# Performance work log

Measured on AMD Instinct MI355X. Metric: run time of the kernel, lower is better.

## Reference

```python
import jax, jax.numpy as jnp
import numpy as np

D_MODEL = 1024
N_HEADS = 16
D_H = D_MODEL // N_HEADS
MAX_LEN = 2048
BATCH = 2
SEQ = 2048
EPS = 1e-8
W_SCALE = 0.02


def _rms_norm(x, w):
    # RMSNorm: x * rsqrt(mean(x^2) + eps) * w
    ms = jnp.mean(jnp.square(x), axis=-1, keepdims=True)
    return w * (x * jax.lax.rsqrt(ms + EPS))


def setup_inputs() -> dict:
    key = jax.random.key(0)
    ks = jax.random.split(key, 12)
    d = D_MODEL
    inp = {
        "x": jax.random.normal(ks[0], (BATCH, SEQ, d), dtype=jnp.float32),
        "t_bias": jnp.zeros((1,), dtype=jnp.float32),  # unused by the module
        "p_bias": jax.random.normal(ks[1], (MAX_LEN, N_HEADS), dtype=jnp.float32),
        # AMS layer params (Linear stored as [in, out])
        "wq": jax.random.normal(ks[2], (d, d), dtype=jnp.float32) * W_SCALE,
        "bq": jnp.zeros((d,), dtype=jnp.float32),
        "wk": jax.random.normal(ks[3], (d, d), dtype=jnp.float32) * W_SCALE,
        "bk": jnp.zeros((d,), dtype=jnp.float32),
        "wv": jax.random.normal(ks[4], (d, d), dtype=jnp.float32) * W_SCALE,
        "bv": jnp.zeros((d,), dtype=jnp.float32),
        "wu": jax.random.normal(ks[5], (d, d), dtype=jnp.float32) * W_SCALE,
        "bu": jnp.zeros((d,), dtype=jnp.float32),
        "g_ams": jnp.ones((d,), dtype=jnp.float32),   # shared RMSNorm weight in AMSLayer
        # MFFN layer params
        "w0": jax.random.normal(ks[6], (d, d), dtype=jnp.float32) * W_SCALE,
        "b0": jnp.zeros((d,), dtype=jnp.float32),
        "w1": jax.random.normal(ks[7], (d, 2 * d), dtype=jnp.float32) * W_SCALE,
        "b1": jnp.zeros((2 * d,), dtype=jnp.float32),
        "w2": jax.random.normal(ks[8], (d, d), dtype=jnp.float32) * W_SCALE,
        "b2": jnp.zeros((d,), dtype=jnp.float32),
        "g_mffn": jnp.ones((d,), dtype=jnp.float32),
    }
    return inp


def reference(x, t_bias, p_bias, wq, bq, wk, bk, wv, bv, wu, bu, g_ams,
              w0, b0, w1, b1, w2, b2, g_mffn):
    B, S, d = x.shape
    H, dh = N_HEADS, D_H

    # ---- AMS layer ----
    x_norm = _rms_norm(x, g_ams)

    def proj(w, b):
        # [B,S,d] -> [B,H,S,dh]
        return (x_norm @ w + b).reshape(B, S, H, dh).transpose(0, 2, 1, 3)

    q = proj(wq, bq)
    k = proj(wk, bk)
    v = proj(wv, bv)

    scale = 1.0 / np.sqrt(dh).astype(np.float32)
    score = jnp.einsum('bhsd,bhtd->bhst', q, k) * scale
    # additive positional bias: p_bias[:S].T -> [H,S], broadcast over query dim
    score = score + p_bias[:S, :].T[None, :, None, :]

    attn = jax.nn.silu(score)                        # SiLU instead of softmax
    out = jnp.einsum('bhst,bhtd->bhsd', attn, v)
    out = out.transpose(0, 2, 1, 3).reshape(B, S, d)

    u = jax.nn.silu(x_norm @ wu + bu)
    ams_out = _rms_norm(out, g_ams) * u

    # ---- MFFN layer ----
    o = (ams_out @ w0 + b0) + x
    o_norm = _rms_norm(o, g_mffn)
    x12 = o_norm @ w1 + b1
    x1, x2 = jnp.split(x12, 2, axis=-1)
    swiglu = jax.nn.silu(x1) * x2
    return (swiglu @ w2 + b2) + o
```

## Files before the change

kernel.cpp:

```cpp
#include <hip/hip_runtime.h>
#include <stdint.h>
#include <math.h>


#define D    1024
#define NH   16
#define DH   64
#define B_   2
#define S_   2048
#define ROWS 4096
#define LQ   4096
#define EPSR 1e-8f

typedef unsigned short u16;
typedef __attribute__((ext_vector_type(8))) short short8;
typedef __attribute__((ext_vector_type(4))) float f32x4;
typedef __attribute__((ext_vector_type(16))) float f32x16;
typedef __attribute__((ext_vector_type(4))) int int4v;

__device__ __forceinline__ float bf2f(u16 u) {
    union { uint32_t i; float f; } c; c.i = ((uint32_t)u) << 16; return c.f;
}
__device__ __forceinline__ u16 f2bf(float f) {
    union { float f; uint32_t i; } c; c.f = f;
    uint32_t x = c.i;
    x += 0x7fffu + ((x >> 16) & 1u);
    return (u16)(x >> 16);
}
#define LOG2E 1.44269504f
__device__ __forceinline__ float silu_fast(float v) {
    return v * __builtin_amdgcn_rcpf(1.0f + __builtin_amdgcn_exp2f(v * -LOG2E));
}

__global__ __launch_bounds__(256) void transpose_all_kernel(
    const float* __restrict__ wq, const float* __restrict__ wk,
    const float* __restrict__ wv, const float* __restrict__ wu,
    const float* __restrict__ w0, const float* __restrict__ w2,
    const float* __restrict__ w1,
    u16* __restrict__ wT4, u16* __restrict__ w0T,
    u16* __restrict__ w2T, u16* __restrict__ w1T)
{
    const unsigned MI = 1u << 20;
    const int z = blockIdx.z;
    const float* W; u16* WT; int N; int noff = 0;
    switch (z) {
        case 0: W = wq; WT = wT4;          N = 1024; break;
        case 1: W = wk; WT = wT4 + 1 * MI; N = 1024; break;
        case 2: W = wv; WT = wT4 + 2 * MI; N = 1024; break;
        case 3: W = wu; WT = wT4 + 3 * MI; N = 1024; break;
        case 4: W = w0; WT = w0T;          N = 1024; break;
        case 5: W = w2; WT = w2T;          N = 1024; break;
        case 6: W = w1; WT = w1T;          N = 2048; noff = 0;    break;
        default:W = w1; WT = w1T;          N = 2048; noff = 1024; break;
    }
    __shared__ float T[64][65];
    const int tid = threadIdx.x;
    const int n0 = (blockIdx.x << 6) + noff;
    const int k0 = blockIdx.y << 6;
    const int rr = tid >> 4;
    const int cc = (tid & 15) << 2;
#pragma unroll
    for (int l = 0; l < 4; ++l) {
        const int r = rr + (l << 4);
        float4 v = *(const float4*)&W[(size_t)(k0 + r) * N + n0 + cc];
        T[cc + 0][r] = v.x; T[cc + 1][r] = v.y;
        T[cc + 2][r] = v.z; T[cc + 3][r] = v.w;
    }
    __syncthreads();
    const int n  = tid >> 2;
    const int ks = (tid & 3) << 4;
#pragma unroll
    for (int m = 0; m < 4; ++m) {
        const int k = ks + (m << 2);
        float4 v = *(const float4*)&T[n][k];
        ushort4 o;
        o.x = f2bf(v.x); o.y = f2bf(v.y); o.z = f2bf(v.z); o.w = f2bf(v.w);
        *(ushort4*)&WT[(size_t)(n0 + n) * 1024 + k0 + k] = o;
    }
}

__global__ __launch_bounds__(256) void pbt_kernel(
    const float* __restrict__ pb, float* __restrict__ pbT)
{
    const int tid = threadIdx.x;
    const int r = (blockIdx.x << 7) + (tid >> 1);
    const int c0 = (tid & 1) << 3;
    float4 v0 = *(const float4*)&pb[(size_t)r * NH + c0];
    float4 v1 = *(const float4*)&pb[(size_t)r * NH + c0 + 4];
    pbT[(size_t)(c0 + 0) * S_ + r] = v0.x;
    pbT[(size_t)(c0 + 1) * S_ + r] = v0.y;
    pbT[(size_t)(c0 + 2) * S_ + r] = v0.z;
    pbT[(size_t)(c0 + 3) * S_ + r] = v0.w;
    pbT[(size_t)(c0 + 4) * S_ + r] = v1.x;
    pbT[(size_t)(c0 + 5) * S_ + r] = v1.y;
    pbT[(size_t)(c0 + 6) * S_ + r] = v1.z;
    pbT[(size_t)(c0 + 7) * S_ + r] = v1.w;
}

__global__ __launch_bounds__(256) void rmsnorm_kernel(
    const float* __restrict__ inf, const u16* __restrict__ inb, int ldi,
    const float* __restrict__ g,
    const u16* __restrict__ mul, int ldm,
    u16* __restrict__ out, int ldo)
{
    const int row = blockIdx.x;
    const int tid = threadIdx.x;
    const int c = tid << 2;
    float x0, x1, x2, x3;
    if (inb) {
        ushort4 xi = *(const ushort4*)&inb[(size_t)row * ldi + c];
        x0 = bf2f(xi.x); x1 = bf2f(xi.y); x2 = bf2f(xi.z); x3 = bf2f(xi.w);
    } else {
        float4 xi = *(const float4*)&inf[(size_t)row * ldi + c];
        x0 = xi.x; x1 = xi.y; x2 = xi.z; x3 = xi.w;
    }
    float ss = x0*x0 + x1*x1 + x2*x2 + x3*x3;
#pragma unroll
    for (int off = 32; off > 0; off >>= 1) ss += __shfl_down(ss, off, 64);
    __shared__ float red[4];
    if ((tid & 63) == 0) red[tid >> 6] = ss;
    __syncthreads();
    float r = rsqrtf((red[0] + red[1] + red[2] + red[3]) * (1.0f / D) + EPSR);
    float4 gv = *(const float4*)&g[c];
    float v0 = x0 * r * gv.x, v1 = x1 * r * gv.y, v2 = x2 * r * gv.z, v3 = x3 * r * gv.w;
    if (mul) {
        ushort4 mi = *(const ushort4*)&mul[(size_t)row * ldm + c];
        v0 *= bf2f(mi.x); v1 *= bf2f(mi.y); v2 *= bf2f(mi.z); v3 *= bf2f(mi.w);
    }
    ushort4 o;
    o.x = f2bf(v0); o.y = f2bf(v1); o.z = f2bf(v2); o.w = f2bf(v3);
    *(ushort4*)&out[(size_t)row * ldo + c] = o;
}

__global__ __launch_bounds__(256) void gemm128(
    const u16* __restrict__ A, const u16* __restrict__ WT,
    const float* __restrict__ bs0, const float* __restrict__ bs1,
    const float* __restrict__ bs2, const float* __restrict__ bs3,
    u16* __restrict__ outb, int ldo, int actmask,
    u16* __restrict__ VT, int vtsel)
{
    __shared__ u16 As[128 * 32];
    __shared__ u16 Bs[128 * 32];
    const int tid  = threadIdx.x;
    const int wave = tid >> 6;
    const int lane = tid & 63;
    const int lm   = lane & 15;
    const int quad = lane >> 4;
    const int row0 = blockIdx.y << 7;
    const int col0 = blockIdx.x << 7;
    const int wr = (wave >> 1) << 6;
    const int wc = (wave & 1) << 6;

    const int srow = wave * 32 + (lane >> 2);
    const int skp  = (lane & 3) << 3;
    const u16* Ag = A  + (size_t)(row0 + srow) * 1024 + skp;
    const u16* Bg = WT + (size_t)(col0 + srow) * 1024 + skp;
    u16* Asd0 = &As[(wave * 32) * 32];
    u16* Asd1 = &As[(wave * 32 + 16) * 32];
    u16* Bsd0 = &Bs[(wave * 32) * 32];
    u16* Bsd1 = &Bs[(wave * 32 + 16) * 32];

    f32x4 acc[4][4] = {};

    for (int k0 = 0; k0 < 1024; k0 += 32) {
        __syncthreads();
        __builtin_amdgcn_global_load_lds(
            (const __attribute__((address_space(1))) void*)(Ag + k0),
            (__attribute__((address_space(3))) void*)Asd0, 16, 0, 0);
        __builtin_amdgcn_global_load_lds(
            (const __attribute__((address_space(1))) void*)(Ag + 16 * 1024 + k0),
            (__attribute__((address_space(3))) void*)Asd1, 16, 0, 0);
        __builtin_amdgcn_global_load_lds(
            (const __attribute__((address_space(1))) void*)(Bg + k0),
            (__attribute__((address_space(3))) void*)Bsd0, 16, 0, 0);
        __builtin_amdgcn_global_load_lds(
            (const __attribute__((address_space(1))) void*)(Bg + 16 * 1024 + k0),
            (__attribute__((address_space(3))) void*)Bsd1, 16, 0, 0);
        __syncthreads();
        short8 af[4], bf[4];
#pragma unroll
        for (int i = 0; i < 4; ++i)
            af[i] = *(const short8*)&As[(wr + i * 16 + lm) * 32 + quad * 8];
#pragma unroll
        for (int j = 0; j < 4; ++j)
            bf[j] = *(const short8*)&Bs[(wc + j * 16 + lm) * 32 + quad * 8];
#pragma unroll
        for (int i = 0; i < 4; ++i)
#pragma unroll
            for (int j = 0; j < 4; ++j)
                acc[i][j] = __builtin_amdgcn_mfma_f32_16x16x32_bf16(af[i], bf[j], acc[i][j], 0, 0, 0);
    }
    const int sel = col0 >> 10;
    const float* bias = (sel == 0) ? bs0 : (sel == 1) ? bs1 : (sel == 2) ? bs2 : bs3;
    const int act = (actmask >> sel) & 1;
    if (VT && sel == vtsel) {
        const int b = row0 >> 11;
#pragma unroll
        for (int j = 0; j < 4; ++j) {
            const int c2 = (col0 + wc + j * 16 + lm) & 1023;
            const int h  = c2 >> 6;
            const int dh = c2 & 63;
            const float bj = bias[c2];
            u16* vrow = VT + ((size_t)(b * NH + h) * 64 + dh) * (size_t)S_;
#pragma unroll
            for (int i = 0; i < 4; ++i) {
                const int tb = (row0 & 2047) + wr + i * 16 + quad * 4;
                ushort4 o;
                o.x = f2bf(acc[i][j][0] + bj);
                o.y = f2bf(acc[i][j][1] + bj);
                o.z = f2bf(acc[i][j][2] + bj);
                o.w = f2bf(acc[i][j][3] + bj);
                *(ushort4*)&vrow[tb] = o;
            }
        }
    } else {
#pragma unroll
        for (int j = 0; j < 4; ++j) {
            const int colg = col0 + wc + j * 16 + lm;
            const float bj = bias[colg & 1023];
#pragma unroll
            for (int i = 0; i < 4; ++i) {
#pragma unroll
                for (int r = 0; r < 4; ++r) {
                    const int rowg = row0 + wr + i * 16 + quad * 4 + r;
                    float v = acc[i][j][r] + bj;
                    if (act) v = silu_fast(v);
                    outb[(size_t)rowg * ldo + colg] = f2bf(v);
                }
            }
        }
    }
}

__global__ __launch_bounds__(256) void gemm64(
    const u16* __restrict__ A, int lda, const u16* __restrict__ WT,
    const float* __restrict__ bias,
    const float* __restrict__ res,
    float* __restrict__ outf, int ldo)
{
    __shared__ u16 As[128 * 32];
    __shared__ u16 Bs[64 * 32];
    const int tid  = threadIdx.x;
    const int wave = tid >> 6;
    const int lane = tid & 63;
    const int lm   = lane & 15;
    const int quad = lane >> 4;
    const int row0 = blockIdx.y << 7;
    const int col0 = blockIdx.x << 6;
    const int wr = (wave >> 1) << 6;
    const int wc = (wave & 1) << 5;

    const int srA = wave * 32 + (lane >> 2);
    const int srB = wave * 16 + (lane >> 2);
    const int skp = (lane & 3) << 3;
    const u16* Ag = A  + (size_t)(row0 + srA) * lda + skp;
    const u16* Bg = WT + (size_t)(col0 + srB) * 1024 + skp;
    u16* Asd0 = &As[(wave * 32) * 32];
    u16* Asd1 = &As[(wave * 32 + 16) * 32];
    u16* Bsd  = &Bs[(wave * 16) * 32];

    f32x4 acc[4][2] = {};

    for (int k0 = 0; k0 < 1024; k0 += 32) {
        __syncthreads();
        __builtin_amdgcn_global_load_lds(
            (const __attribute__((address_space(1))) void*)(Ag + k0),
            (__attribute__((address_space(3))) void*)Asd0, 16, 0, 0);
        __builtin_amdgcn_global_load_lds(
            (const __attribute__((address_space(1))) void*)(Ag + (size_t)16 * lda + k0),
            (__attribute__((address_space(3))) void*)Asd1, 16, 0, 0);
        __builtin_amdgcn_global_load_lds(
            (const __attribute__((address_space(1))) void*)(Bg + k0),
            (__attribute__((address_space(3))) void*)Bsd, 16, 0, 0);
        __syncthreads();
        short8 af[4], bf[2];
#pragma unroll
        for (int i = 0; i < 4; ++i)
            af[i] = *(const short8*)&As[(wr + i * 16 + lm) * 32 + quad * 8];
#pragma unroll
        for (int j = 0; j < 2; ++j)
            bf[j] = *(const short8*)&Bs[(wc + j * 16 + lm) * 32 + quad * 8];
#pragma unroll
        for (int i = 0; i < 4; ++i)
#pragma unroll
            for (int j = 0; j < 2; ++j)
                acc[i][j] = __builtin_amdgcn_mfma_f32_16x16x32_bf16(af[i], bf[j], acc[i][j], 0, 0, 0);
    }
#pragma unroll
    for (int j = 0; j < 2; ++j) {
        const int colg = col0 + wc + j * 16 + lm;
        const float bj = bias[colg];
#pragma unroll
        for (int i = 0; i < 4; ++i) {
#pragma unroll
            for (int r = 0; r < 4; ++r) {
                const int rowg = row0 + wr + i * 16 + quad * 4 + r;
                const size_t idx = (size_t)rowg * ldo + colg;
                float v = acc[i][j][r] + bj;
                if (res) v += res[idx];
                outf[idx] = v;
            }
        }
    }
}

__global__ __launch_bounds__(512, 2) void attn_mfma(
    const u16* __restrict__ qkvu, const u16* __restrict__ VT,
    const float* __restrict__ pbT, u16* __restrict__ out)
{
    __shared__ u16 Ks[2][2][64 * 64];
    __shared__ u16 Vs[2][2][64 * 64];
    __shared__ float pbl[S_];
    const int tid  = threadIdx.x;
    const int wave = tid >> 6;
    const int grp  = wave >> 2;
    const int wq4  = wave & 3;
    const int lane = tid & 63;
    const int l31  = lane & 31;
    const int hi   = lane >> 5;
    const int l7   = lane & 7;
    const int flat = blockIdx.x + (blockIdx.y << 4) + (blockIdx.z << 8);
    const int work = ((flat & 7) << 6) + (flat >> 3);
    const int s0 = (work & 15) << 7;
    const int h  = (work >> 4) & 15;
    const int b  = work >> 8;
    const size_t base = (size_t)b * S_ * LQ + (size_t)h * DH;
    const u16* q  = qkvu + base;
    const u16* kg = qkvu + base + 1024;
    const u16* vt = VT + (size_t)(b * NH + h) * 64 * S_;
    const float* pbh = pbT + (size_t)h * S_;

    for (int i = tid * 4; i < S_; i += 2048)
        *(float4*)&pbl[i] = *(const float4*)&pbh[i];

    const int qrow = s0 + wq4 * 32 + l31;
    short8 qf[4];
#pragma unroll
    for (int i = 0; i < 4; ++i)
        qf[i] = *(const short8*)&q[(size_t)qrow * LQ + i * 16 + hi * 8];

    const int lr  = lane >> 3;
    const int gch = l7 ^ lr;
    const u16* kg0 = kg + (size_t)(16 * wq4 + lr) * LQ + gch * 8;
    const u16* vg0 = vt + (size_t)(16 * wq4 + lr) * S_ + gch * 8;

#define GLDS(gp, lp) __builtin_amdgcn_global_load_lds( \
        (const __attribute__((address_space(1))) void*)(gp), \
        (__attribute__((address_space(3))) void*)(lp), 16, 0, 0)
#define ISSUE(it, bu) do { \
        const size_t tn = ((size_t)(grp) * 16 + (size_t)(it)) << 6; \
        GLDS(kg0 + tn * LQ,             &Ks[grp][bu][(16 * wq4) * 64]); \
        GLDS(kg0 + (tn + 8) * LQ,       &Ks[grp][bu][(16 * wq4 + 8) * 64]); \
        GLDS(vg0 + tn,                  &Vs[grp][bu][(16 * wq4) * 64]); \
        GLDS(vg0 + tn + (size_t)8 * S_, &Vs[grp][bu][(16 * wq4 + 8) * 64]); \
    } while (0)

    f32x16 accO[2] = {};
    ISSUE(0, 0);
    __syncthreads();

#pragma unroll 1
    for (int it = 0; it < 16; ++it) {
        const int ib = it & 1;
        const int nb = ib ^ 1;
        if (it + 1 < 16) ISSUE(it + 1, nb);
        const int t0 = grp * 1024 + (it << 6);
#pragma unroll
        for (int half = 0; half < 2; ++half) {
            const int ts = half << 5;
            f32x16 st = {};
            __builtin_amdgcn_s_setprio(1);
#pragma unroll
            for (int i = 0; i < 4; ++i) {
                short8 kf = *(const short8*)&Ks[grp][ib][(ts + l31) * 64 + (((2 * i + hi) ^ l7) << 3)];
                st = __builtin_amdgcn_mfma_f32_32x32x16_bf16(kf, qf[i], st, 0, 0, 0);
            }
            __builtin_amdgcn_s_setprio(0);
            int pk[8];
#pragma unroll
            for (int g = 0; g < 4; ++g) {
                float4 pbv = *(const float4*)&pbl[t0 + ts + 8 * g + 4 * hi];
                float p0 = silu_fast(fmaf(st[4 * g + 0], 0.125f, pbv.x));
                float p1 = silu_fast(fmaf(st[4 * g + 1], 0.125f, pbv.y));
                float p2 = silu_fast(fmaf(st[4 * g + 2], 0.125f, pbv.z));
                float p3 = silu_fast(fmaf(st[4 * g + 3], 0.125f, pbv.w));
                asm("v_cvt_pk_bf16_f32 %0, %1, %2" : "=v"(pk[2 * g])     : "v"(p0), "v"(p1));
                asm("v_cvt_pk_bf16_f32 %0, %1, %2" : "=v"(pk[2 * g + 1]) : "v"(p2), "v"(p3));
            }
#pragma unroll
            for (int m = 0; m < 2; ++m) {
                int w0 = pk[4 * m + 0], w2 = pk[4 * m + 2];
                int w1 = pk[4 * m + 1], w3 = pk[4 * m + 3];
                asm("v_permlane32_swap_b32 %0, %1" : "+v"(w0), "+v"(w2));
                asm("v_permlane32_swap_b32 %0, %1" : "+v"(w1), "+v"(w3));
                union { int4v i; short8 s; } pa;
                pa.i.x = w0; pa.i.y = w1; pa.i.z = w2; pa.i.w = w3;
                __builtin_amdgcn_s_setprio(1);
#pragma unroll
                for (int n = 0; n < 2; ++n) {
                    short8 vf = *(const short8*)&Vs[grp][ib][(32 * n + l31) * 64 +
                        ((((ts >> 3) + 2 * m + hi) ^ l7) << 3)];
                    accO[n] = __builtin_amdgcn_mfma_f32_32x32x16_bf16(pa.s, vf, accO[n], 0, 0, 0);
                }
                __builtin_amdgcn_s_setprio(0);
            }
        }
        __syncthreads();
    }
#undef ISSUE
#undef GLDS
    float* scr = (float*)&Ks[0][0][0];
    const int sl = wq4 * 64 + lane;
    if (grp == 1) {
#pragma unroll
        for (int n = 0; n < 2; ++n)
#pragma unroll
            for (int r = 0; r < 16; ++r)
                scr[(n * 16 + r) * 256 + sl] = accO[n][r];
    }
    __syncthreads();
    if (grp == 0) {
#pragma unroll
        for (int n = 0; n < 2; ++n)
#pragma unroll
            for (int r = 0; r < 16; ++r)
                accO[n][r] += scr[(n * 16 + r) * 256 + sl];
        const int qb = s0 + wq4 * 32 + 4 * hi;
#pragma unroll
        for (int n = 0; n < 2; ++n)
#pragma unroll
            for (int r = 0; r < 16; ++r) {
                const int qq = qb + (r & 3) + 8 * (r >> 2);
                out[base + (size_t)qq * LQ + 32 * n + l31] = f2bf(accO[n][r]);
            }
    }
}

__global__ __launch_bounds__(256) void swiglu_kernel(u16* __restrict__ qkvu)
{
    const size_t e = ((size_t)blockIdx.x * 256 + threadIdx.x) << 2;
    const size_t r = e >> 10;
    const int    c = (int)(e & 1023);
    ushort4 a = *(const ushort4*)&qkvu[r * LQ + c];
    ushort4 b = *(const ushort4*)&qkvu[r * LQ + 1024 + c];
    ushort4 o;
    o.x = f2bf(silu_fast(bf2f(a.x)) * bf2f(b.x));
    o.y = f2bf(silu_fast(bf2f(a.y)) * bf2f(b.y));
    o.z = f2bf(silu_fast(bf2f(a.z)) * bf2f(b.z));
    o.w = f2bf(silu_fast(bf2f(a.w)) * bf2f(b.w));
    *(ushort4*)&qkvu[r * LQ + 2048 + c] = o;
}

extern "C" void kernel_launch(void* const* d_in, const int* in_sizes, int n_in,
                              void* d_out, int out_size, void* d_ws, size_t ws_size,
                              hipStream_t stream)
{
    const float* x      = (const float*)d_in[0];
    const float* pb     = (const float*)d_in[2];
    const float* wq     = (const float*)d_in[3];
    const float* bq     = (const float*)d_in[4];
    const float* wk     = (const float*)d_in[5];
    const float* bk     = (const float*)d_in[6];
    const float* wv     = (const float*)d_in[7];
    const float* bv     = (const float*)d_in[8];
    const float* wu     = (const float*)d_in[9];
    const float* bu     = (const float*)d_in[10];
    const float* g_ams  = (const float*)d_in[11];
    const float* w0     = (const float*)d_in[12];
    const float* b0     = (const float*)d_in[13];
    const float* w1     = (const float*)d_in[14];
    const float* b1     = (const float*)d_in[15];
    const float* w2     = (const float*)d_in[16];
    const float* b2     = (const float*)d_in[17];
    const float* g_mffn = (const float*)d_in[18];
    float* OUT = (float*)d_out;
    u16*   VT  = (u16*)d_out;
    float* pbT = (float*)((u16*)d_out + 4 * (1u << 20));

    const size_t MI = 1024 * 1024;
    u16* WS   = (u16*)d_ws;
    u16* wT4  = WS;
    u16* w0T  = WS + 4 * MI;
    u16* w2T  = WS + 5 * MI;
    u16* w1T  = WS + 6 * MI;
    u16* A0   = WS + 8 * MI;
    u16* QKVU = WS + 12 * MI;

    dim3 blk(256);

    transpose_all_kernel<<<dim3(16, 16, 8), blk, 0, stream>>>(
        wq, wk, wv, wu, w0, w2, w1, wT4, w0T, w2T, w1T);
    pbt_kernel<<<16, blk, 0, stream>>>(pb, pbT);

    rmsnorm_kernel<<<ROWS, blk, 0, stream>>>(x, nullptr, D, g_ams, nullptr, 0, A0, D);
    gemm128<<<dim3(32, 32), blk, 0, stream>>>(A0, wT4, bq, bk, bv, bu,
                                              QKVU, LQ, 0b1000, VT, 2);
    attn_mfma<<<dim3(16, 16, 2), dim3(512), 0, stream>>>(QKVU, VT, pbT, QKVU);
    rmsnorm_kernel<<<ROWS, blk, 0, stream>>>(nullptr, QKVU, LQ, g_ams, QKVU + 3072, LQ, A0, D);
    gemm64<<<dim3(16, 32), blk, 0, stream>>>(A0, D, w0T, b0, x, OUT, D);
    rmsnorm_kernel<<<ROWS, blk, 0, stream>>>(OUT, nullptr, D, g_mffn, nullptr, 0, A0, D);
    gemm128<<<dim3(16, 32), blk, 0, stream>>>(A0, w1T, b1, b1 + 1024, b1, b1,
                                              QKVU, LQ, 0, nullptr, -1);
    swiglu_kernel<<<ROWS * D / 1024, blk, 0, stream>>>(QKVU);
    gemm64<<<dim3(16, 32), blk, 0, stream>>>(QKVU + 2048, LQ, w2T, b2, OUT, OUT, D);
    (void)ws_size; (void)in_sizes; (void)n_in; (void)out_size;
}
```

Before: 330.6 us.

## Fuse W1 GEMM with SwiGLU epilogue and restructure attention K/V swizzle

Adds a dedicated W1 GEMM that computes matching x1 and x2 column tiles in one block and applies silu(x1)*x2 in the epilogue. This removes the separate swiglu kernel and the round trip of the full x12 intermediate through memory. The attention kernel also changes its LDS XOR swizzle and processes both 32-key halves together, which gives more independent MFMAs per iteration. That should improve latency hiding and reduce LDS bank conflicts, at the cost of more registers.

```diff
diff --git a/kernel.cpp b/kernel.cpp
--- a/kernel.cpp
+++ b/kernel.cpp
@@ -304,6 +304,82 @@
     }
 }
 
+__global__ __launch_bounds__(256) void gemm_w1_swiglu(
+    const u16* __restrict__ A, const u16* __restrict__ WT,
+    const float* __restrict__ b1, u16* __restrict__ outb)
+{
+    __shared__ u16 As[128 * 32];
+    __shared__ u16 Bs[128 * 32];
+    const int tid  = threadIdx.x;
+    const int wave = tid >> 6;
+    const int lane = tid & 63;
+    const int lm   = lane & 15;
+    const int quad = lane >> 4;
+    const int row0 = blockIdx.y << 7;
+    const int col0 = blockIdx.x << 6;
+    const int wr  = (wave >> 1) << 6;
+    const int wc2 = (wave & 1) << 5;
+
+    const int srow = wave * 32 + (lane >> 2);
+    const int skp  = (lane & 3) << 3;
+    const int brow = col0 + (srow & 63) + ((srow >> 6) << 10);
+    const u16* Ag = A  + (size_t)(row0 + srow) * 1024 + skp;
+    const u16* Bg = WT + (size_t)brow * 1024 + skp;
+    u16* Asd0 = &As[(wave * 32) * 32];
+    u16* Asd1 = &As[(wave * 32 + 16) * 32];
+    u16* Bsd0 = &Bs[(wave * 32) * 32];
+    u16* Bsd1 = &Bs[(wave * 32 + 16) * 32];
+
+    f32x4 acc[4][4] = {};
+
+    for (int k0 = 0; k0 < 1024; k0 += 32) {
+        __syncthreads();
+        __builtin_amdgcn_global_load_lds(
+            (const __attribute__((address_space(1))) void*)(Ag + k0),
+            (__attribute__((address_space(3))) void*)Asd0, 16, 0, 0);
+        __builtin_amdgcn_global_load_lds(
+            (const __attribute__((address_space(1))) void*)(Ag + 16 * 1024 + k0),
+            (__attribute__((address_space(3))) void*)Asd1, 16, 0, 0);
+        __builtin_amdgcn_global_load_lds(
+            (const __attribute__((address_space(1))) void*)(Bg + k0),
+            (__attribute__((address_space(3))) void*)Bsd0, 16, 0, 0);
+        __builtin_amdgcn_global_load_lds(
+            (const __attribute__((address_space(1))) void*)(Bg + 16 * 1024 + k0),
+            (__attribute__((address_space(3))) void*)Bsd1, 16, 0, 0);
+        __syncthreads();
+        short8 af[4], bf[4];
+#pragma unroll
+        for (int i = 0; i < 4; ++i)
+            af[i] = *(const short8*)&As[(wr + i * 16 + lm) * 32 + quad * 8];
+#pragma unroll
+        for (int j = 0; j < 2; ++j) {
+            bf[j]     = *(const short8*)&Bs[(wc2 + j * 16 + lm) * 32 + quad * 8];
+            bf[j + 2] = *(const short8*)&Bs[(64 + wc2 + j * 16 + lm) * 32 + quad * 8];
+        }
+#pragma unroll
+        for (int i = 0; i < 4; ++i)
+#pragma unroll
+            for (int j = 0; j < 4; ++j)
+                acc[i][j] = __builtin_amdgcn_mfma_f32_16x16x32_bf16(af[i], bf[j], acc[i][j], 0, 0, 0);
+    }
+#pragma unroll
+    for (int j = 0; j < 2; ++j) {
+        const int colg = col0 + wc2 + j * 16 + lm;
+        const float ba = b1[colg];
+        const float bb = b1[1024 + colg];
+#pragma unroll
+        for (int i = 0; i < 4; ++i) {
+#pragma unroll
+            for (int r = 0; r < 4; ++r) {
+                const int rowg = row0 + wr + i * 16 + quad * 4 + r;
+                const float x1v = acc[i][j][r] + ba;
+                const float x2v = acc[i][j + 2][r] + bb;
+                outb[(size_t)rowg * LQ + colg] = f2bf(silu_fast(x1v) * x2v);
+            }
+        }
+    }
+}
+
 __global__ __launch_bounds__(512, 2) void attn_mfma(
     const u16* __restrict__ qkvu, const u16* __restrict__ VT,
     const float* __restrict__ pbT, u16* __restrict__ out)
@@ -319,6 +395,7 @@
     const int l31  = lane & 31;
     const int hi   = lane >> 5;
     const int l7   = lane & 7;
+    const int xorv = l7 ^ ((l31 >> 3) & 3);
     const int flat = blockIdx.x + (blockIdx.y << 4) + (blockIdx.z << 8);
     const int work = ((flat & 7) << 6) + (flat >> 3);
     const int s0 = (work & 15) << 7;
@@ -340,19 +417,22 @@
         qf[i] = *(const short8*)&q[(size_t)qrow * LQ + i * 16 + hi * 8];
 
     const int lr  = lane >> 3;
-    const int gch = l7 ^ lr;
-    const u16* kg0 = kg + (size_t)(16 * wq4 + lr) * LQ + gch * 8;
-    const u16* vg0 = vt + (size_t)(16 * wq4 + lr) * S_ + gch * 8;
+    const int gA  = (2 * wq4) & 3;
+    const int gB  = (2 * wq4 + 1) & 3;
+    const u16* kgA = kg + (size_t)(16 * wq4 + lr) * LQ     + ((l7 ^ lr ^ gA) << 3);
+    const u16* kgB = kg + (size_t)(16 * wq4 + 8 + lr) * LQ + ((l7 ^ lr ^ gB) << 3);
+    const u16* vgA = vt + (size_t)(16 * wq4 + lr) * S_     + ((l7 ^ lr ^ gA) << 3);
+    const u16* vgB = vt + (size_t)(16 * wq4 + 8 + lr) * S_ + ((l7 ^ lr ^ gB) << 3);
 
 #define GLDS(gp, lp) __builtin_amdgcn_global_load_lds( \
         (const __attribute__((address_space(1))) void*)(gp), \
         (__attribute__((address_space(3))) void*)(lp), 16, 0, 0)
 #define ISSUE(it, bu) do { \
         const size_t tn = ((size_t)(grp) * 16 + (size_t)(it)) << 6; \
-        GLDS(kg0 + tn * LQ,             &Ks[grp][bu][(16 * wq4) * 64]); \
-        GLDS(kg0 + (tn + 8) * LQ,       &Ks[grp][bu][(16 * wq4 + 8) * 64]); \
-        GLDS(vg0 + tn,                  &Vs[grp][bu][(16 * wq4) * 64]); \
-        GLDS(vg0 + tn + (size_t)8 * S_, &Vs[grp][bu][(16 * wq4 + 8) * 64]); \
+        GLDS(kgA + tn * LQ, &Ks[grp][bu][(16 * wq4) * 64]); \
+        GLDS(kgB + tn * LQ, &Ks[grp][bu][(16 * wq4 + 8) * 64]); \
+        GLDS(vgA + tn,      &Vs[grp][bu][(16 * wq4) * 64]); \
+        GLDS(vgB + tn,      &Vs[grp][bu][(16 * wq4 + 8) * 64]); \
     } while (0)
 
     f32x16 accO[2] = {};
@@ -365,45 +445,59 @@
         const int nb = ib ^ 1;
         if (it + 1 < 16) ISSUE(it + 1, nb);
         const int t0 = grp * 1024 + (it << 6);
-#pragma unroll
-        for (int half = 0; half < 2; ++half) {
-            const int ts = half << 5;
-            f32x16 st = {};
+        f32x16 st0 = {}, st1 = {};
+        __builtin_amdgcn_s_setprio(1);
+#pragma unroll
+        for (int i = 0; i < 4; ++i) {
+            const int co = ((2 * i + hi) ^ xorv) << 3;
+            short8 kf0 = *(const short8*)&Ks[grp][ib][(l31) * 64 + co];
+            short8 kf1 = *(const short8*)&Ks[grp][ib][(32 + l31) * 64 + co];
+            st0 = __builtin_amdgcn_mfma_f32_32x32x16_bf16(kf0, qf[i], st0, 0, 0, 0);
+            st1 = __builtin_amdgcn_mfma_f32_32x32x16_bf16(kf1, qf[i], st1, 0, 0, 0);
+        }
+        __builtin_amdgcn_s_setprio(0);
+        int pk0[8], pk1[8];
+#pragma unroll
+        for (int g = 0; g < 4; ++g) {
+            float4 pbv0 = *(const float4*)&pbl[t0 + 8 * g + 4 * hi];
+            float4 pbv1 = *(const float4*)&pbl[t0 + 32 + 8 * g + 4 * hi];
+            float a0 = silu_fast(fmaf(st0[4 * g + 0], 0.125f, pbv0.x));
+            float a1 = silu_fast(fmaf(st0[4 * g + 1], 0.125f, pbv0.y));
+            float a2 = silu_fast(fmaf(st0[4 * g + 2], 0.125f, pbv0.z));
+            float a3 = silu_fast(fmaf(st0[4 * g + 3], 0.125f, pbv0.w));
+            float b0 = silu_fast(fmaf(st1[4 * g + 0], 0.125f, pbv1.x));
+            float b1 = silu_fast(fmaf(st1[4 * g + 1], 0.125f, pbv1.y));
+            float b2 = silu_fast(fmaf(st1[4 * g + 2], 0.125f, pbv1.z));
+            float b3 = silu_fast(fmaf(st1[4 * g + 3], 0.125f, pbv1.w));
+            asm("v_cvt_pk_bf16_f32 %0, %1, %2" : "=v"(pk0[2 * g])     : "v"(a0), "v"(a1));
+            asm("v_cvt_pk_bf16_f32 %0, %1, %2" : "=v"(pk0[2 * g + 1]) : "v"(a2), "v"(a3));
+            asm("v_cvt_pk_bf16_f32 %0, %1, %2" : "=v"(pk1[2 * g])     : "v"(b0), "v"(b1));
+            asm("v_cvt_pk_bf16_f32 %0, %1, %2" : "=v"(pk1[2 * g + 1]) : "v"(b2), "v"(b3));
+        }
+#pragma unroll
+        for (int m = 0; m < 2; ++m) {
+            int w0 = pk0[4 * m + 0], w2 = pk0[4 * m + 2];
+            int w1 = pk0[4 * m + 1], w3 = pk0[4 * m + 3];
+            asm("v_permlane32_swap_b32 %0, %1" : "+v"(w0), "+v"(w2));
+            asm("v_permlane32_swap_b32 %0, %1" : "+v"(w1), "+v"(w3));
+            int u0 = pk1[4 * m + 0], u2 = pk1[4 * m + 2];
+            int u1 = pk1[4 * m + 1], u3 = pk1[4 * m + 3];
+            asm("v_permlane32_swap_b32 %0, %1" : "+v"(u0), "+v"(u2));
+            asm("v_permlane32_swap_b32 %0, %1" : "+v"(u1), "+v"(u3));
+            union { int4v i; short8 s; } pa, pb2;
+            pa.i.x  = w0; pa.i.y  = w1; pa.i.z  = w2; pa.i.w  = w3;
+            pb2.i.x = u0; pb2.i.y = u1; pb2.i.z = u2; pb2.i.w = u3;
             __builtin_amdgcn_s_setprio(1);
 #pragma unroll
-            for (int i = 0; i < 4; ++i) {
-                short8 kf = *(const short8*)&Ks[grp][ib][(ts + l31) * 64 + (((2 * i + hi) ^ l7) << 3)];
-                st = __builtin_amdgcn_mfma_f32_32x32x16_bf16(kf, qf[i], st, 0, 0, 0);
+            for (int n = 0; n < 2; ++n) {
+                short8 vf0 = *(const short8*)&Vs[grp][ib][(32 * n + l31) * 64 +
+                    (((2 * m + hi) ^ xorv) << 3)];
+                short8 vf1 = *(const short8*)&Vs[grp][ib][(32 * n + l31) * 64 +
+                    (((4 + 2 * m + hi) ^ xorv) << 3)];
+                accO[n] = __builtin_amdgcn_mfma_f32_32x32x16_bf16(pa.s,  vf0, accO[n], 0, 0, 0);
+                accO[n] = __builtin_amdgcn_mfma_f32_32x32x16_bf16(pb2.s, vf1, accO[n], 0, 0, 0);
             }
             __builtin_amdgcn_s_setprio(0);
-            int pk[8];
-#pragma unroll
-            for (int g = 0; g < 4; ++g) {
-                float4 pbv = *(const float4*)&pbl[t0 + ts + 8 * g + 4 * hi];
-                float p0 = silu_fast(fmaf(st[4 * g + 0], 0.125f, pbv.x));
-                float p1 = silu_fast(fmaf(st[4 * g + 1], 0.125f, pbv.y));
-                float p2 = silu_fast(fmaf(st[4 * g + 2], 0.125f, pbv.z));
-                float p3 = silu_fast(fmaf(st[4 * g + 3], 0.125f, pbv.w));
-                asm("v_cvt_pk_bf16_f32 %0, %1, %2" : "=v"(pk[2 * g])     : "v"(p0), "v"(p1));
-                asm("v_cvt_pk_bf16_f32 %0, %1, %2" : "=v"(pk[2 * g + 1]) : "v"(p2), "v"(p3));
-            }
-#pragma unroll
-            for (int m = 0; m < 2; ++m) {
-                int w0 = pk[4 * m + 0], w2 = pk[4 * m + 2];
-                int w1 = pk[4 * m + 1], w3 = pk[4 * m + 3];
-                asm("v_permlane32_swap_b32 %0, %1" : "+v"(w0), "+v"(w2));
-                asm("v_permlane32_swap_b32 %0, %1" : "+v"(w1), "+v"(w3));
-                union { int4v i; short8 s; } pa;
-                pa.i.x = w0; pa.i.y = w1; pa.i.z = w2; pa.i.w = w3;
-                __builtin_amdgcn_s_setprio(1);
-#pragma unroll
-                for (int n = 0; n < 2; ++n) {
-                    short8 vf = *(const short8*)&Vs[grp][ib][(32 * n + l31) * 64 +
-                        ((((ts >> 3) + 2 * m + hi) ^ l7) << 3)];
-                    accO[n] = __builtin_amdgcn_mfma_f32_32x32x16_bf16(pa.s, vf, accO[n], 0, 0, 0);
-                }
-                __builtin_amdgcn_s_setprio(0);
-            }
         }
         __syncthreads();
     }
@@ -434,21 +528,6 @@
                 out[base + (size_t)qq * LQ + 32 * n + l31] = f2bf(accO[n][r]);
             }
     }
-}
-
-__global__ __launch_bounds__(256) void swiglu_kernel(u16* __restrict__ qkvu)
-{
-    const size_t e = ((size_t)blockIdx.x * 256 + threadIdx.x) << 2;
-    const size_t r = e >> 10;
-    const int    c = (int)(e & 1023);
-    ushort4 a = *(const ushort4*)&qkvu[r * LQ + c];
-    ushort4 b = *(const ushort4*)&qkvu[r * LQ + 1024 + c];
-    ushort4 o;
-    o.x = f2bf(silu_fast(bf2f(a.x)) * bf2f(b.x));
-    o.y = f2bf(silu_fast(bf2f(a.y)) * bf2f(b.y));
-    o.z = f2bf(silu_fast(bf2f(a.z)) * bf2f(b.z));
-    o.w = f2bf(silu_fast(bf2f(a.w)) * bf2f(b.w));
-    *(ushort4*)&qkvu[r * LQ + 2048 + c] = o;
 }
 
 extern "C" void kernel_launch(void* const* d_in, const int* in_sizes, int n_in,
@@ -499,9 +578,7 @@
     rmsnorm_kernel<<<ROWS, blk, 0, stream>>>(nullptr, QKVU, LQ, g_ams, QKVU + 3072, LQ, A0, D);
     gemm64<<<dim3(16, 32), blk, 0, stream>>>(A0, D, w0T, b0, x, OUT, D);
     rmsnorm_kernel<<<ROWS, blk, 0, stream>>>(OUT, nullptr, D, g_mffn, nullptr, 0, A0, D);
-    gemm128<<<dim3(16, 32), blk, 0, stream>>>(A0, w1T, b1, b1 + 1024, b1, b1,
-                                              QKVU, LQ, 0, nullptr, -1);
-    swiglu_kernel<<<ROWS * D / 1024, blk, 0, stream>>>(QKVU);
+    gemm_w1_swiglu<<<dim3(16, 32), blk, 0, stream>>>(A0, w1T, b1, QKVU + 2048);
     gemm64<<<dim3(16, 32), blk, 0, stream>>>(QKVU + 2048, LQ, w2T, b2, OUT, OUT, D);
     (void)ws_size; (void)in_sizes; (void)n_in; (void)out_size;
 }
```

Measured after the change: 322.2 us. 1.03x faster.
